# Optimization experiments

Hardware: AMD Instinct MI355X
Metric: run time of the kernel (lower is better)

## Reference

```python
import jax, jax.numpy as jnp
import numpy as np

N = 50000      # nodes
E = 800000     # edges
IN_CH = 32
H = 64         # hidden_channels
OUT_CH = 16
L = 4          # num_layers
EPS = 1e-7     # GENConv message eps
LN_EPS = 1e-5


def _lin(key, fan_in, fan_out):
    kw, kb = jax.random.split(key)
    s = 1.0 / np.sqrt(fan_in)
    W = jax.random.uniform(kw, (fan_in, fan_out), jnp.float32, -s, s)
    b = jax.random.uniform(kb, (fan_out,), jnp.float32, -s, s)
    return W, b


def setup_inputs() -> dict:
    key = jax.random.key(0)
    ks = jax.random.split(key, 8)
    x = jax.random.normal(ks[0], (N, IN_CH), jnp.float32)
    edge_index = jax.random.randint(ks[1], (2, E), 0, N, dtype=jnp.int32)
    node_W, node_b = _lin(ks[2], IN_CH, H)
    W1, b1, W2, b2 = [], [], [], []
    for i in range(L):
        w1, bb1 = _lin(jax.random.fold_in(ks[3], i), H, 2 * H)
        w2, bb2 = _lin(jax.random.fold_in(ks[4], i), 2 * H, H)
        W1.append(w1); b1.append(bb1); W2.append(w2); b2.append(bb2)
    inp = {
        "x": x,
        "node_W": node_W, "node_b": node_b,
        "W1": jnp.stack(W1), "b1": jnp.stack(b1),          # [L,H,2H],[L,2H]
        "mlp_ln_g": jnp.ones((L, 2 * H), jnp.float32),      # LayerNorm inside GENConv MLP
        "mlp_ln_b": jnp.zeros((L, 2 * H), jnp.float32),
        "W2": jnp.stack(W2), "b2": jnp.stack(b2),          # [L,2H,H],[L,H]
        "t": jnp.ones((L,), jnp.float32),                   # learnable softmax temperature
        "ln_g": jnp.ones((L, H), jnp.float32),              # DeepGCNLayer LayerNorms
        "ln_b": jnp.zeros((L, H), jnp.float32),
        "edge_index": edge_index,
    }
    gW, gb = _lin(ks[5], H, OUT_CH)
    nW, nb = _lin(ks[6], H, OUT_CH + 1)
    inp.update({"g_W": gW, "g_b": gb, "n_W": nW, "n_b": nb})
    return inp


def _layer_norm(h, g, b):
    mu = h.mean(-1, keepdims=True)
    var = ((h - mu) ** 2).mean(-1, keepdims=True)
    return (h - mu) * jax.lax.rsqrt(var + LN_EPS) * g + b


def _gen_conv(h, src, dst, W1, b1, lg, lb, W2, b2, t):
    # message: relu(x_j) + eps  -> [E, H]
    m = jax.nn.relu(h[src]) + EPS
    # per-destination, per-channel scatter softmax with temperature t
    z = t * m
    zmax = jax.ops.segment_max(z, dst, num_segments=N)
    zmax = jnp.where(jnp.isfinite(zmax), zmax, 0.0)  # empty segments -> -inf
    a = jnp.exp(z - zmax[dst])
    denom = jax.ops.segment_sum(a, dst, num_segments=N)
    agg = jax.ops.segment_sum(m * a, dst, num_segments=N) / jnp.maximum(denom, EPS)
    out = agg + h  # root add
    # MLP [H, 2H, H] with LayerNorm + ReLU between
    u = jax.nn.relu(_layer_norm(out @ W1 + b1, lg, lb))
    return u @ W2 + b2


def reference(x, node_W, node_b, W1, b1, mlp_ln_g, mlp_ln_b, W2, b2, t,
              ln_g, ln_b, g_W, g_b, n_W, n_b, edge_index):
    src, dst = edge_index[0], edge_index[1]
    h = x @ node_W + node_b  # node encoder
    # first layer: conv only
    h = _gen_conv(h, src, dst, W1[0], b1[0], mlp_ln_g[0], mlp_ln_b[0], W2[0], b2[0], t[0])
    # remaining res+ blocks: x + conv(relu(norm(x)))  (dropout identity in eval)
    for i in range(1, L):
        y = jax.nn.relu(_layer_norm(h, ln_g[i], ln_b[i]))
        h = h + _gen_conv(y, src, dst, W1[i], b1[i], mlp_ln_g[i], mlp_ln_b[i], W2[i], b2[i], t[i])
    h = jax.nn.relu(_layer_norm(h, ln_g[0], ln_b[0]))
    g_out = jnp.max(h @ g_W + g_b, axis=0)   # batch=None -> global max over nodes
    n_out = h @ n_W + n_b
    return g_out, n_out
```

## Files before the change

kernel.cpp:

```cpp
#include <hip/hip_runtime.h>

#define NN 50000
#define NE 800000
#define INC 32
#define HH 64
#define H2 128
#define OC 16
#define ON 17
#define NL 4
#define MEPS 1e-7f
#define LNE 1e-5f
#define SCAN_BLOCKS 196
#define NMB ((NN + 127) / 128)
#define NBW ((NL * H2 * HH + 255) / 256)
#define NBH4 ((NE + 1023) / 1024)
#define NBE8 ((NN + 7) / 8)

typedef __attribute__((ext_vector_type(8))) short bf16x8;
typedef __attribute__((ext_vector_type(4))) float f32x4;

__device__ __forceinline__ unsigned short f2b(float x) {
    unsigned b = __float_as_uint(x);
    b += 0x7FFFu + ((b >> 16) & 1u);
    return (unsigned short)(b >> 16);
}
__device__ __forceinline__ float b2f(unsigned short u) {
    return __uint_as_float(((unsigned)u) << 16);
}

__global__ __launch_bounds__(256) void k_pre(
    const float* __restrict__ W1, const float* __restrict__ W2,
    const float* __restrict__ nW, const float* __restrict__ gW,
    const float* __restrict__ nbp, const float* __restrict__ gb,
    unsigned short* __restrict__ w1h, unsigned short* __restrict__ w1l,
    unsigned short* __restrict__ w2h, unsigned short* __restrict__ w2l,
    unsigned short* __restrict__ whh, unsigned short* __restrict__ whl,
    float* __restrict__ bc,
    const int* __restrict__ edst, int* __restrict__ counts, int* __restrict__ rank,
    const float* __restrict__ x, const float* __restrict__ nodeW,
    const float* __restrict__ nodeB, float* __restrict__ h,
    unsigned short* __restrict__ hbf)
{
    __shared__ float Ws[INC * HH];
    __shared__ float bs[HH];
    int bid = blockIdx.x, tid = threadIdx.x;
    if (bid < NBW) {
        int i = bid * 256 + tid;
        if (i < 48 * 64) {
            int j = i >> 6, k = i & 63;
            float v = 0.f;
            if (j < ON) v = nW[k * ON + j];
            else if (j < 33) v = gW[k * OC + (j - ON)];
            unsigned short hi = f2b(v);
            whh[i] = hi;
            whl[i] = f2b(v - b2f(hi));
        }
        if (i < 48) bc[i] = (i < ON) ? nbp[i] : ((i < 33) ? gb[i - ON] : 0.f);
        if (i >= NL * H2 * HH) return;
        int l = i / (H2 * HH), r = i % (H2 * HH);
        {
            int c = r / HH, k = r % HH;
            float v = W1[(size_t)l * HH * H2 + (size_t)k * H2 + c];
            unsigned short hi = f2b(v);
            w1h[i] = hi;
            w1l[i] = f2b(v - b2f(hi));
        }
        {
            int c = r / H2, k = r % H2;
            float v = W2[(size_t)l * H2 * HH + (size_t)k * HH + c];
            unsigned short hi = f2b(v);
            w2h[i] = hi;
            w2l[i] = f2b(v - b2f(hi));
        }
        return;
    }
    if (bid < NBW + NBH4) {
        int base = (bid - NBW) * 1024 + tid;
        #pragma unroll
        for (int k = 0; k < 4; ++k) {
            int e = base + k * 256;
            if (e < NE) rank[e] = atomicAdd(&counts[edst[e]], 1);
        }
        return;
    }
    for (int i = tid; i < INC * HH; i += 256) Ws[i] = nodeW[i];
    if (tid < HH) bs[tid] = nodeB[tid];
    __syncthreads();
    int wid = tid >> 6, lane = tid & 63;
    int n0 = (bid - NBW - NBH4) * 8 + wid * 2;
    int n1 = n0 + 1;
    bool v0ok = n0 < NN, v1ok = n1 < NN;
    if (!v0ok) return;
    float v0 = (lane < INC) ? x[(size_t)n0 * INC + lane] : 0.f;
    float v1 = (v1ok && lane < INC) ? x[(size_t)n1 * INC + lane] : 0.f;
    float a0 = bs[lane], a1 = a0;
    #pragma unroll
    for (int k = 0; k < INC; ++k) {
        float wv = Ws[k * HH + lane];
        a0 += __shfl(v0, k) * wv;
        a1 += __shfl(v1, k) * wv;
    }
    h[(size_t)n0 * HH + lane] = a0;
    hbf[(size_t)n0 * HH + lane] = f2b(a0);
    if (v1ok) {
        h[(size_t)n1 * HH + lane] = a1;
        hbf[(size_t)n1 * HH + lane] = f2b(a1);
    }
}

__global__ __launch_bounds__(256) void k_scan1(const int* __restrict__ counts,
                                               int* __restrict__ incl, int* __restrict__ bsums) {
    __shared__ int s[256];
    int t = threadIdx.x;
    int i = blockIdx.x * 256 + t;
    int v = (i < NN) ? counts[i] : 0;
    s[t] = v;
    __syncthreads();
    for (int off = 1; off < 256; off <<= 1) {
        int x = (t >= off) ? s[t - off] : 0;
        __syncthreads();
        s[t] += x;
        __syncthreads();
    }
    if (i < NN) incl[i] = s[t];
    if (t == 255) bsums[blockIdx.x] = s[255];
}

__global__ __launch_bounds__(256) void k_scan23(const int* __restrict__ counts,
                                                int* __restrict__ rowst, const int* __restrict__ bsums,
                                                int2* __restrict__ meta) {
    __shared__ int s[256];
    int t = threadIdx.x;
    int v = (t < SCAN_BLOCKS) ? bsums[t] : 0;
    s[t] = v;
    __syncthreads();
    for (int off = 1; off < 256; off <<= 1) {
        int x = (t >= off) ? s[t - off] : 0;
        __syncthreads();
        s[t] += x;
        __syncthreads();
    }
    int ex = s[t] - v;
    __syncthreads();
    s[t] = ex;
    __syncthreads();
    int pref = s[blockIdx.x];
    int i = blockIdx.x * 256 + t;
    if (i < NN) {
        int st = rowst[i] - counts[i] + pref;
        rowst[i] = st;
        meta[i] = make_int2(st, counts[i]);
    }
}

__global__ __launch_bounds__(256) void k_scatter2(const int* __restrict__ src, const int* __restrict__ dst,
                                                  const int* __restrict__ rank, const int* __restrict__ rowst,
                                                  int* __restrict__ ssrc) {
    int base = blockIdx.x * 1024 + threadIdx.x;
    #pragma unroll
    for (int k = 0; k < 4; ++k) {
        int e = base + k * 256;
        if (e < NE) ssrc[rowst[dst[e]] + rank[e]] = src[e];
    }
}

__global__ __launch_bounds__(256) void k_agg(const float* __restrict__ y,
                                             const unsigned short* __restrict__ ybf,
                                             const int2* __restrict__ meta,
                                             const int* __restrict__ ssrc,
                                             const float* __restrict__ tp,
                                             unsigned short* __restrict__ agh,
                                             unsigned short* __restrict__ agl) {
    int tid = threadIdx.x;
    int w = tid >> 6, lane = tid & 63;
    int half = lane >> 5;
    int l = lane & 31;
    int col = l;
    int n = blockIdx.x * 8 + w * 2 + half;
    bool valid = n < NN;
    float tval = *tp;
    int2 m = valid ? meta[n] : make_int2(0, 0);
    int start = m.x, deg = m.y;

    int dA = __shfl(deg, 0), dB = __shfl(deg, 32);
    int dmax = max(dA, dB);

    float Sa0 = 0.f, Sm0 = 0.f, Sa1 = 0.f, Sm1 = 0.f;
    for (int win = 0; win < dmax; win += 64) {
        int wcnt = min(64, dmax - win);
        int idxLo = (win + l < deg) ? ssrc[start + win + l] : 0;
        int idxHi = (win + 32 + l < deg) ? ssrc[start + win + 32 + l] : 0;
        for (int e0 = 0; e0 < wcnt; e0 += 8) {
            float c0[8], c1[8];
            int ev[8];
            #pragma unroll
            for (int i = 0; i < 8; ++i) {
                int e = e0 + i;
                ev[i] = win + e;
                int sel = (e < 32) ? idxLo : idxHi;
                int s = __shfl(sel, (lane & 32) | (e & 31));
                unsigned v = *(const unsigned*)(ybf + (size_t)s * HH + col * 2);
                c0[i] = b2f((unsigned short)(v & 0xffffu));
                c1[i] = b2f((unsigned short)(v >> 16));
            }
            #pragma unroll
            for (int i = 0; i < 8; ++i) {
                bool ok = ev[i] < deg;
                float m0 = fmaxf(c0[i], 0.f) + MEPS;
                float m1 = fmaxf(c1[i], 0.f) + MEPS;
                float a0 = ok ? __expf(tval * m0) : 0.f;
                float a1 = ok ? __expf(tval * m1) : 0.f;
                Sa0 += a0; Sm0 += m0 * a0;
                Sa1 += a1; Sm1 += m1 * a1;
            }
        }
    }
    if (!valid) return;
    float agg0 = Sm0 / fmaxf(Sa0, MEPS);
    float agg1 = Sm1 / fmaxf(Sa1, MEPS);
    float2 yv = *(const float2*)(y + (size_t)n * HH + col * 2);
    float av0 = agg0 + yv.x;
    float av1 = agg1 + yv.y;
    unsigned short h0 = f2b(av0), h1 = f2b(av1);
    ushort2 ph = {h0, h1};
    ushort2 pl = {f2b(av0 - b2f(h0)), f2b(av1 - b2f(h1))};
    *(ushort2*)(agh + (size_t)n * HH + col * 2) = ph;
    *(ushort2*)(agl + (size_t)n * HH + col * 2) = pl;
}

__global__ __launch_bounds__(512, 4) void k_mlp(
    const unsigned short* __restrict__ agh, const unsigned short* __restrict__ agl,
    const unsigned short* __restrict__ w1h, const unsigned short* __restrict__ w1l,
    const float* __restrict__ b1,
    const float* __restrict__ mlg, const float* __restrict__ mlb,
    const unsigned short* __restrict__ w2h, const unsigned short* __restrict__ w2l,
    const float* __restrict__ b2,
    const float* __restrict__ hres, float* __restrict__ hout,
    const float* __restrict__ lng1, const float* __restrict__ lnb1,
    float* __restrict__ y, unsigned short* __restrict__ ybf,
    const float* __restrict__ lngF, const float* __restrict__ lnbF,
    const unsigned short* __restrict__ whh, const unsigned short* __restrict__ whl,
    const float* __restrict__ bc, float* __restrict__ dout, float* __restrict__ gmax)
{
    __shared__ __align__(16) unsigned short W1S[2 * 128 * 72];
    __shared__ __align__(16) unsigned short W2hS[64 * 136];
    __shared__ __align__(16) unsigned short W2lS[64 * 136];
    __shared__ float smax[8][16];
    bool last = (lng1 == nullptr);
    int tid = threadIdx.x;
    int w = tid >> 6, lane = tid & 63;
    int nl = lane & 15, g = lane >> 4;
    int node = blockIdx.x * 128 + w * 16 + nl;
    bool valid = node < NN;

    bf16x8 bAh[2], bAl[2];
    {
        bf16x8 z = {0, 0, 0, 0, 0, 0, 0, 0};
        if (valid) {
            const unsigned short* rp = agh + (size_t)node * HH + g * 8;
            bAh[0] = *(const bf16x8*)rp;
            bAh[1] = *(const bf16x8*)(rp + 32);
            const unsigned short* rq = agl + (size_t)node * HH + g * 8;
            bAl[0] = *(const bf16x8*)rq;
            bAl[1] = *(const bf16x8*)(rq + 32);
        } else {
            bAh[0] = z; bAh[1] = z; bAl[0] = z; bAl[1] = z;
        }
    }

    #pragma unroll
    for (int it = 0; it < 2; ++it) {
        int c = tid + it * 512;
        int row = c >> 3, col = (c & 7) << 3;
        float4 vh = *(const float4*)(w1h + c * 8);
        float4 vl = *(const float4*)(w1l + c * 8);
        *(float4*)&W1S[row * 72 + col] = vh;
        *(float4*)&W1S[9216 + row * 72 + col] = vl;
    }
    #pragma unroll
    for (int it = 0; it < 2; ++it) {
        int c = tid + it * 512;
        int row = c >> 4, col = (c & 15) << 3;
        float4 vh = *(const float4*)(w2h + c * 8);
        float4 vl = *(const float4*)(w2l + c * 8);
        *(float4*)&W2hS[row * 136 + col] = vh;
        *(float4*)&W2lS[row * 136 + col] = vl;
    }
    __syncthreads();

    f32x4 accU[8];
    #pragma unroll
    for (int t = 0; t < 8; ++t) {
        int uc = t * 16 + g * 4;
        float4 bb = *(const float4*)(b1 + uc);
        f32x4 a = {bb.x, bb.y, bb.z, bb.w};
        #pragma unroll
        for (int kc = 0; kc < 2; ++kc) {
            int wo = (t * 16 + nl) * 72 + kc * 32 + g * 8;
            bf16x8 ah = *(const bf16x8*)&W1S[wo];
            bf16x8 al = *(const bf16x8*)&W1S[9216 + wo];
            a = __builtin_amdgcn_mfma_f32_16x16x32_bf16(ah, bAh[kc], a, 0, 0, 0);
            a = __builtin_amdgcn_mfma_f32_16x16x32_bf16(al, bAh[kc], a, 0, 0, 0);
            a = __builtin_amdgcn_mfma_f32_16x16x32_bf16(ah, bAl[kc], a, 0, 0, 0);
        }
        accU[t] = a;
    }

    float s = 0.f, sq = 0.f;
    #pragma unroll
    for (int t = 0; t < 8; ++t) {
        #pragma unroll
        for (int j = 0; j < 4; ++j) { float v = accU[t][j]; s += v; sq += v * v; }
    }
    s += __shfl_xor(s, 16); sq += __shfl_xor(sq, 16);
    s += __shfl_xor(s, 32); sq += __shfl_xor(sq, 32);
    float mu = s * (1.f / 128.f);
    float var = sq * (1.f / 128.f) - mu * mu;
    float rs = rsqrtf(fmaxf(var, 0.f) + LNE);

    __syncthreads();
    unsigned short* myUt = W1S + w * (16 * 136);

    #pragma unroll
    for (int t = 0; t < 8; ++t) {
        int uc = t * 16 + g * 4;
        float4 gg = *(const float4*)(mlg + uc);
        float4 bb = *(const float4*)(mlb + uc);
        ushort4 pk;
        pk.x = f2b(fmaxf((accU[t][0] - mu) * rs * gg.x + bb.x, 0.f));
        pk.y = f2b(fmaxf((accU[t][1] - mu) * rs * gg.y + bb.y, 0.f));
        pk.z = f2b(fmaxf((accU[t][2] - mu) * rs * gg.z + bb.z, 0.f));
        pk.w = f2b(fmaxf((accU[t][3] - mu) * rs * gg.w + bb.w, 0.f));
        *(ushort4*)(&myUt[nl * 136 + uc]) = pk;
    }
    asm volatile("s_waitcnt lgkmcnt(0)" ::: "memory");

    bf16x8 bB[4];
    #pragma unroll
    for (int kc = 0; kc < 4; ++kc)
        bB[kc] = *(const bf16x8*)(&myUt[nl * 136 + kc * 32 + g * 8]);

    f32x4 accO[4];
    #pragma unroll
    for (int ot = 0; ot < 4; ++ot) {
        int oc = ot * 16 + g * 4;
        float4 bb = *(const float4*)(b2 + oc);
        f32x4 a = {bb.x, bb.y, bb.z, bb.w};
        #pragma unroll
        for (int kc = 0; kc < 4; ++kc) {
            int wo = (ot * 16 + nl) * 136 + kc * 32 + g * 8;
            bf16x8 ah = *(const bf16x8*)&W2hS[wo];
            bf16x8 al = *(const bf16x8*)&W2lS[wo];
            a = __builtin_amdgcn_mfma_f32_16x16x32_bf16(ah, bB[kc], a, 0, 0, 0);
            a = __builtin_amdgcn_mfma_f32_16x16x32_bf16(al, bB[kc], a, 0, 0, 0);
        }
        accO[ot] = a;
    }

    float4 oo[4];
    #pragma unroll
    for (int ot = 0; ot < 4; ++ot) {
        int oc = ot * 16 + g * 4;
        float4 o;
        o.x = accO[ot][0]; o.y = accO[ot][1]; o.z = accO[ot][2]; o.w = accO[ot][3];
        if (valid && hres) {
            float4 hr = *(const float4*)(hres + (size_t)node * HH + oc);
            o.x += hr.x; o.y += hr.y; o.z += hr.z; o.w += hr.w;
        }
        oo[ot] = o;
    }

    float s2 = 0.f, sq2 = 0.f;
    #pragma unroll
    for (int ot = 0; ot < 4; ++ot) {
        s2 += oo[ot].x + oo[ot].y + oo[ot].z + oo[ot].w;
        sq2 += oo[ot].x * oo[ot].x + oo[ot].y * oo[ot].y
             + oo[ot].z * oo[ot].z + oo[ot].w * oo[ot].w;
    }
    s2 += __shfl_xor(s2, 16); sq2 += __shfl_xor(sq2, 16);
    s2 += __shfl_xor(s2, 32); sq2 += __shfl_xor(sq2, 32);
    float mu2 = s2 * (1.f / 64.f);
    float var2 = sq2 * (1.f / 64.f) - mu2 * mu2;
    float rs2 = rsqrtf(fmaxf(var2, 0.f) + LNE);

    if (!last) {
        #pragma unroll
        for (int ot = 0; ot < 4; ++ot) {
            int oc = ot * 16 + g * 4;
            if (valid) *(float4*)(hout + (size_t)node * HH + oc) = oo[ot];
        }
        #pragma unroll
        for (int ot = 0; ot < 4; ++ot) {
            int oc = ot * 16 + g * 4;
            float4 gg = *(const float4*)(lng1 + oc);
            float4 bb = *(const float4*)(lnb1 + oc);
            float4 v;
            v.x = fmaxf((oo[ot].x - mu2) * rs2 * gg.x + bb.x, 0.f);
            v.y = fmaxf((oo[ot].y - mu2) * rs2 * gg.y + bb.y, 0.f);
            v.z = fmaxf((oo[ot].z - mu2) * rs2 * gg.z + bb.z, 0.f);
            v.w = fmaxf((oo[ot].w - mu2) * rs2 * gg.w + bb.w, 0.f);
            if (valid) {
                *(float4*)(y + (size_t)node * HH + oc) = v;
                ushort4 p;
                p.x = f2b(v.x); p.y = f2b(v.y); p.z = f2b(v.z); p.w = f2b(v.w);
                *(ushort4*)(ybf + (size_t)node * HH + oc) = p;
            }
        }
        return;
    }

    union { bf16x8 v; unsigned short u[8]; } Bh[2], Bl[2];
    #pragma unroll
    for (int kc = 0; kc < 2; ++kc) {
        #pragma unroll
        for (int e = 0; e < 8; ++e) {
            int ot = kc * 2 + (e >> 2);
            int c = ot * 16 + g * 4 + (e & 3);
            float hv = (e & 3) == 0 ? oo[ot].x : ((e & 3) == 1 ? oo[ot].y : ((e & 3) == 2 ? oo[ot].z : oo[ot].w));
            float v = fmaxf((hv - mu2) * rs2 * lngF[c] + lnbF[c], 0.f);
            unsigned short hi = f2b(v);
            Bh[kc].u[e] = hi;
            Bl[kc].u[e] = f2b(v - b2f(hi));
        }
    }
    f32x4 acc[3];
    #pragma unroll
    for (int t = 0; t < 3; ++t) {
        int j0 = t * 16 + g * 4;
        float4 bb = *(const float4*)(bc + j0);
        f32x4 a = {bb.x, bb.y, bb.z, bb.w};
        #pragma unroll
        for (int kc = 0; kc < 2; ++kc) {
            union { bf16x8 v; unsigned short u[8]; } Ah, Al;
            #pragma unroll
            for (int e = 0; e < 8; ++e) {
                int ot = kc * 2 + (e >> 2);
                int c = ot * 16 + g * 4 + (e & 3);
                Ah.u[e] = whh[(size_t)(t * 16 + nl) * 64 + c];
                Al.u[e] = whl[(size_t)(t * 16 + nl) * 64 + c];
            }
            a = __builtin_amdgcn_mfma_f32_16x16x32_bf16(Ah.v, Bh[kc].v, a, 0, 0, 0);
            a = __builtin_amdgcn_mfma_f32_16x16x32_bf16(Al.v, Bh[kc].v, a, 0, 0, 0);
            a = __builtin_amdgcn_mfma_f32_16x16x32_bf16(Ah.v, Bl[kc].v, a, 0, 0, 0);
        }
        acc[t] = a;
    }

    #pragma unroll
    for (int t = 0; t < 3; ++t) {
        #pragma unroll
        for (int reg = 0; reg < 4; ++reg) {
            int j = t * 16 + g * 4 + reg;
            float val = acc[t][reg];
            if (j < ON) {
                if (valid) dout[OC + (size_t)node * ON + j] = val;
            } else if (j < 33) {
                float gv = valid ? val : -INFINITY;
                #pragma unroll
                for (int m = 1; m < 16; m <<= 1) gv = fmaxf(gv, __shfl_xor(gv, m));
                if (nl == 0) smax[w][j - ON] = gv;
            }
        }
    }
    __syncthreads();
    if (tid < 16) {
        float mm = -INFINITY;
        #pragma unroll
        for (int ww = 0; ww < 8; ++ww) mm = fmaxf(mm, smax[ww][tid]);
        gmax[(size_t)blockIdx.x * 16 + tid] = mm;
    }
}

__global__ void k_gdec(const float* __restrict__ gmax, float* __restrict__ dout) {
    int lane = threadIdx.x & 63;
    int ch = lane & 15, grp = lane >> 4;
    float m = -INFINITY;
    for (int b = grp; b < NMB; b += 4) m = fmaxf(m, gmax[(size_t)b * 16 + ch]);
    m = fmaxf(m, __shfl_xor(m, 16));
    m = fmaxf(m, __shfl_xor(m, 32));
    if (lane < 16) dout[ch] = m;
}

extern "C" void kernel_launch(void* const* d_in, const int* in_sizes, int n_in,
                              void* d_out, int out_size, void* d_ws, size_t ws_size,
                              hipStream_t stream) {
    const float* x     = (const float*)d_in[0];
    const float* nodeW = (const float*)d_in[1];
    const float* nodeB = (const float*)d_in[2];
    const float* W1    = (const float*)d_in[3];
    const float* b1    = (const float*)d_in[4];
    const float* mlg   = (const float*)d_in[5];
    const float* mlb   = (const float*)d_in[6];
    const float* W2    = (const float*)d_in[7];
    const float* b2    = (const float*)d_in[8];
    const float* tt    = (const float*)d_in[9];
    const float* lng   = (const float*)d_in[10];
    const float* lnb   = (const float*)d_in[11];
    const int*   ei    = (const int*)d_in[12];
    const float* gW    = (const float*)d_in[13];
    const float* gb    = (const float*)d_in[14];
    const float* nW    = (const float*)d_in[15];
    const float* nbp   = (const float*)d_in[16];
    float* out = (float*)d_out;

    char* ws = (char*)d_ws;
    size_t off = 0;
    auto alloc = [&](size_t bytes) -> void* {
        void* p = ws + off;
        off = (off + bytes + 255) & ~(size_t)255;
        return p;
    };
    int* counts    = (int*)alloc((size_t)NN * 4);
    size_t zero_end = off;
    float* gmax = (float*)alloc((size_t)NMB * 16 * 4);
    int* bsums = (int*)alloc(1024);
    int* rowst = (int*)alloc((size_t)NN * 4);
    int2* meta = (int2*)alloc((size_t)NN * 8);
    int* ssrc  = (int*)alloc((size_t)NE * 4);
    float* h   = (float*)alloc((size_t)NN * HH * 4);
    float* y   = (float*)alloc((size_t)NN * HH * 4);
    unsigned short* agh = (unsigned short*)alloc((size_t)NN * HH * 2);
    unsigned short* agl = (unsigned short*)alloc((size_t)NN * HH * 2);
    unsigned short* ybf = (unsigned short*)alloc((size_t)NN * HH * 2);
    unsigned short* w1h = (unsigned short*)alloc((size_t)NL * H2 * HH * 2);
    unsigned short* w1l = (unsigned short*)alloc((size_t)NL * H2 * HH * 2);
    unsigned short* w2h = (unsigned short*)alloc((size_t)NL * H2 * HH * 2);
    unsigned short* w2l = (unsigned short*)alloc((size_t)NL * H2 * HH * 2);
    unsigned short* whh = (unsigned short*)alloc((size_t)48 * 64 * 2);
    unsigned short* whl = (unsigned short*)alloc((size_t)48 * 64 * 2);
    float* bc = (float*)alloc(48 * 4);
    int* rank = (int*)agh;

    const int* esrc = ei;
    const int* edst = ei + NE;

    hipMemsetAsync(d_ws, 0, zero_end, stream);

    k_pre<<<NBW + NBH4 + NBE8, 256, 0, stream>>>(W1, W2, nW, gW, nbp, gb,
                                                 w1h, w1l, w2h, w2l, whh, whl, bc,
                                                 edst, counts, rank,
                                                 x, nodeW, nodeB, h, ybf);
    k_scan1<<<SCAN_BLOCKS, 256, 0, stream>>>(counts, rowst, bsums);
    k_scan23<<<SCAN_BLOCKS, 256, 0, stream>>>(counts, rowst, bsums, meta);
    k_scatter2<<<(NE + 1023) / 1024, 256, 0, stream>>>(esrc, edst, rank, rowst, ssrc);

    for (int l = 0; l < NL; ++l) {
        const float* yin = (l == 0) ? h : y;
        k_agg<<<(NN + 7) / 8, 256, 0, stream>>>(yin, ybf, meta, ssrc, tt + l, agh, agl);
        bool lastL = (l == NL - 1);
        const float* ln1g = lastL ? nullptr : (lng + (size_t)(l + 1) * HH);
        const float* ln1b = lastL ? nullptr : (lnb + (size_t)(l + 1) * HH);
        k_mlp<<<NMB, 512, 0, stream>>>(agh, agl,
                                       w1h + (size_t)l * H2 * HH, w1l + (size_t)l * H2 * HH,
                                       b1 + (size_t)l * H2,
                                       mlg + (size_t)l * H2, mlb + (size_t)l * H2,
                                       w2h + (size_t)l * H2 * HH, w2l + (size_t)l * H2 * HH,
                                       b2 + (size_t)l * HH,
                                       (l == 0) ? (const float*)nullptr : h, h,
                                       ln1g, ln1b, y, ybf,
                                       lng, lnb, whh, whl, bc, out, gmax);
    }
    k_gdec<<<1, 64, 0, stream>>>(gmax, out);
}
```

Baseline: 372.3 us.

## Replace global-atomic CSR build with two-level bucket sort by destination

Edges are no longer counted with global atomics on 50k per-node counters. They are first bucketed by dst>>8 using LDS histograms per 1024-edge block, then a single-block scan computes bucket offsets, edges are scattered as (src,dst) pairs into buckets, and a per-bucket kernel does an LDS counting sort to produce ssrc and meta. This removes the memset and contended global atomics. In exchange it adds an extra pass over the edges and a serial single-block scan over about 196x782 histogram entries. The order of edges within a node may now differ from before.

```diff
diff --git a/kernel.cpp b/kernel.cpp
--- a/kernel.cpp
+++ b/kernel.cpp
@@ -10,11 +10,11 @@
 #define NL 4
 #define MEPS 1e-7f
 #define LNE 1e-5f
-#define SCAN_BLOCKS 196
 #define NMB ((NN + 127) / 128)
 #define NBW ((NL * H2 * HH + 255) / 256)
 #define NBH4 ((NE + 1023) / 1024)
 #define NBE8 ((NN + 7) / 8)
+#define NBK  ((NN + 255) / 256)
 
 typedef __attribute__((ext_vector_type(8))) short bf16x8;
 typedef __attribute__((ext_vector_type(4))) float f32x4;
@@ -36,13 +36,14 @@
     unsigned short* __restrict__ w2h, unsigned short* __restrict__ w2l,
     unsigned short* __restrict__ whh, unsigned short* __restrict__ whl,
     float* __restrict__ bc,
-    const int* __restrict__ edst, int* __restrict__ counts, int* __restrict__ rank,
+    const int* __restrict__ edst, int* __restrict__ bhist, unsigned short* __restrict__ lrank,
     const float* __restrict__ x, const float* __restrict__ nodeW,
     const float* __restrict__ nodeB, float* __restrict__ h,
     unsigned short* __restrict__ hbf)
 {
     __shared__ float Ws[INC * HH];
     __shared__ float bs[HH];
+    __shared__ int histS[256];
     int bid = blockIdx.x, tid = threadIdx.x;
     if (bid < NBW) {
         int i = bid * 256 + tid;
@@ -75,12 +76,20 @@
         return;
     }
     if (bid < NBW + NBH4) {
-        int base = (bid - NBW) * 1024 + tid;
+        int blk = bid - NBW;
+        histS[tid] = 0;
+        __syncthreads();
+        int base = blk * 1024 + tid;
         #pragma unroll
         for (int k = 0; k < 4; ++k) {
             int e = base + k * 256;
-            if (e < NE) rank[e] = atomicAdd(&counts[edst[e]], 1);
-        }
+            if (e < NE) {
+                int r = atomicAdd(&histS[edst[e] >> 8], 1);
+                lrank[e] = (unsigned short)r;
+            }
+        }
+        __syncthreads();
+        if (tid < NBK) bhist[tid * NBH4 + blk] = histS[tid];
         return;
     }
     for (int i = tid; i < INC * HH; i += 256) Ws[i] = nodeW[i];
@@ -108,13 +117,19 @@
     }
 }
 
-__global__ __launch_bounds__(256) void k_scan1(const int* __restrict__ counts,
-                                               int* __restrict__ incl, int* __restrict__ bsums) {
+__global__ __launch_bounds__(256) void k_bscan(int* __restrict__ bhist,
+                                               int* __restrict__ bbase, int* __restrict__ btot) {
     __shared__ int s[256];
     int t = threadIdx.x;
-    int i = blockIdx.x * 256 + t;
-    int v = (i < NN) ? counts[i] : 0;
-    s[t] = v;
+    int run = 0;
+    if (t < NBK) {
+        for (int blk = 0; blk < NBH4; ++blk) {
+            int v = bhist[t * NBH4 + blk];
+            bhist[t * NBH4 + blk] = run;
+            run += v;
+        }
+    }
+    s[t] = (t < NBK) ? run : 0;
     __syncthreads();
     for (int off = 1; off < 256; off <<= 1) {
         int x = (t >= off) ? s[t - off] : 0;
@@ -122,17 +137,42 @@
         s[t] += x;
         __syncthreads();
     }
-    if (i < NN) incl[i] = s[t];
-    if (t == 255) bsums[blockIdx.x] = s[255];
-}
-
-__global__ __launch_bounds__(256) void k_scan23(const int* __restrict__ counts,
-                                                int* __restrict__ rowst, const int* __restrict__ bsums,
-                                                int2* __restrict__ meta) {
-    __shared__ int s[256];
-    int t = threadIdx.x;
-    int v = (t < SCAN_BLOCKS) ? bsums[t] : 0;
-    s[t] = v;
+    if (t < NBK) {
+        bbase[t] = s[t] - run;
+        btot[t] = run;
+    }
+}
+
+__global__ __launch_bounds__(256) void k_bscatter(const int* __restrict__ src, const int* __restrict__ dst,
+                                                  const unsigned short* __restrict__ lrank,
+                                                  const int* __restrict__ bhist, const int* __restrict__ bbase,
+                                                  int2* __restrict__ pairs) {
+    int blk = blockIdx.x;
+    int base = blk * 1024 + threadIdx.x;
+    #pragma unroll
+    for (int k = 0; k < 4; ++k) {
+        int e = base + k * 256;
+        if (e < NE) {
+            int d = dst[e];
+            int b = d >> 8;
+            int pos = bbase[b] + bhist[b * NBH4 + blk] + (int)lrank[e];
+            pairs[pos] = make_int2(src[e], d);
+        }
+    }
+}
+
+__global__ __launch_bounds__(256) void k_bsort(const int2* __restrict__ pairs,
+                                               const int* __restrict__ bbase, const int* __restrict__ btot,
+                                               int* __restrict__ ssrc, int2* __restrict__ meta) {
+    __shared__ int cnt[256], s[256], cur[256];
+    int b = blockIdx.x, t = threadIdx.x;
+    int S = bbase[b], L = btot[b];
+    cnt[t] = 0;
+    __syncthreads();
+    for (int i = S + t; i < S + L; i += 256) atomicAdd(&cnt[pairs[i].y & 255], 1);
+    __syncthreads();
+    int c = cnt[t];
+    s[t] = c;
     __syncthreads();
     for (int off = 1; off < 256; off <<= 1) {
         int x = (t >= off) ? s[t - off] : 0;
@@ -140,27 +180,15 @@
         s[t] += x;
         __syncthreads();
     }
-    int ex = s[t] - v;
-    __syncthreads();
-    s[t] = ex;
-    __syncthreads();
-    int pref = s[blockIdx.x];
-    int i = blockIdx.x * 256 + t;
-    if (i < NN) {
-        int st = rowst[i] - counts[i] + pref;
-        rowst[i] = st;
-        meta[i] = make_int2(st, counts[i]);
-    }
-}
-
-__global__ __launch_bounds__(256) void k_scatter2(const int* __restrict__ src, const int* __restrict__ dst,
-                                                  const int* __restrict__ rank, const int* __restrict__ rowst,
-                                                  int* __restrict__ ssrc) {
-    int base = blockIdx.x * 1024 + threadIdx.x;
-    #pragma unroll
-    for (int k = 0; k < 4; ++k) {
-        int e = base + k * 256;
-        if (e < NE) ssrc[rowst[dst[e]] + rank[e]] = src[e];
+    int sst = s[t] - c;
+    cur[t] = sst;
+    int node = b * 256 + t;
+    if (node < NN) meta[node] = make_int2(S + sst, c);
+    __syncthreads();
+    for (int i = S + t; i < S + L; i += 256) {
+        int2 p = pairs[i];
+        int pos = atomicAdd(&cur[p.y & 255], 1);
+        ssrc[S + pos] = p.x;
     }
 }
 
@@ -510,11 +538,10 @@
         off = (off + bytes + 255) & ~(size_t)255;
         return p;
     };
-    int* counts    = (int*)alloc((size_t)NN * 4);
-    size_t zero_end = off;
+    int* bhist = (int*)alloc((size_t)NBK * NBH4 * 4);
+    int* bbase = (int*)alloc((size_t)NBK * 4);
+    int* btot  = (int*)alloc((size_t)NBK * 4);
     float* gmax = (float*)alloc((size_t)NMB * 16 * 4);
-    int* bsums = (int*)alloc(1024);
-    int* rowst = (int*)alloc((size_t)NN * 4);
     int2* meta = (int2*)alloc((size_t)NN * 8);
     int* ssrc  = (int*)alloc((size_t)NE * 4);
     float* h   = (float*)alloc((size_t)NN * HH * 4);
@@ -529,20 +556,19 @@
     unsigned short* whh = (unsigned short*)alloc((size_t)48 * 64 * 2);
     unsigned short* whl = (unsigned short*)alloc((size_t)48 * 64 * 2);
     float* bc = (float*)alloc(48 * 4);
-    int* rank = (int*)agh;
+    unsigned short* lrank = (unsigned short*)agh;
+    int2* pairs = (int2*)y;
 
     const int* esrc = ei;
     const int* edst = ei + NE;
 
-    hipMemsetAsync(d_ws, 0, zero_end, stream);
-
     k_pre<<<NBW + NBH4 + NBE8, 256, 0, stream>>>(W1, W2, nW, gW, nbp, gb,
                                                  w1h, w1l, w2h, w2l, whh, whl, bc,
-                                                 edst, counts, rank,
+                                                 edst, bhist, lrank,
                                                  x, nodeW, nodeB, h, ybf);
-    k_scan1<<<SCAN_BLOCKS, 256, 0, stream>>>(counts, rowst, bsums);
-    k_scan23<<<SCAN_BLOCKS, 256, 0, stream>>>(counts, rowst, bsums, meta);
-    k_scatter2<<<(NE + 1023) / 1024, 256, 0, stream>>>(esrc, edst, rank, rowst, ssrc);
+    k_bscan<<<1, 256, 0, stream>>>(bhist, bbase, btot);
+    k_bscatter<<<NBH4, 256, 0, stream>>>(esrc, edst, lrank, bhist, bbase, pairs);
+    k_bsort<<<NBK, 256, 0, stream>>>(pairs, bbase, btot, ssrc, meta);
 
     for (int l = 0; l < NL; ++l) {
         const float* yin = (l == 0) ? h : y;
```

Measured after the change: 406.3 us. 9.1% more time.
